# Performance work log

Hardware: AMD Instinct MI355X
Metric: run time of the kernel (lower is better)

## Reference

```python
import jax, jax.numpy as jnp
import numpy as np

B, L, D, H, R = 2, 2048, 1024, 16, 512
HD = D // H  # head dim = 64
EPS = 1e-5


def layernorm(x, g, b):
    mu = jnp.mean(x, axis=-1, keepdims=True)
    var = jnp.mean(jnp.square(x - mu), axis=-1, keepdims=True)
    return (x - mu) * jax.lax.rsqrt(var + EPS) * g + b


def rel_pos_bias(res_pos, size):
    # Equivalent to the torch 'skew' causal_mask: bias[h, i, j] = res_pos[h, i-j]
    # if 0 <= i-j < R else -inf (causal + clipped relative distance).
    d = jnp.arange(size)[:, None] - jnp.arange(size)[None, :]  # (L, L)
    valid = (d >= 0) & (d < res_pos.shape[-1])
    gathered = res_pos[:, jnp.clip(d, 0, res_pos.shape[-1] - 1)]  # (H, L, L)
    return jnp.where(valid, gathered, -jnp.inf)


def setup_inputs() -> dict:
    key = jax.random.key(0)
    ks = jax.random.split(key, 12)
    s = lambda fan: 1.0 / np.sqrt(fan)
    return {
        "x": jax.random.normal(ks[0], (B, L, D), jnp.float32),
        "res_pos": jax.random.normal(ks[1], (H, R), jnp.float32) * 0.02,
        "w_qkv": jax.random.normal(ks[2], (D, 3 * D), jnp.float32) * s(D),
        "b_qkv": jnp.zeros((3 * D,), jnp.float32),
        "w_out": jax.random.normal(ks[3], (D, D), jnp.float32) * s(D),
        "b_out": jnp.zeros((D,), jnp.float32),
        "w1": jax.random.normal(ks[4], (D, 4 * D), jnp.float32) * s(D),
        "b1": jnp.zeros((4 * D,), jnp.float32),
        "w2": jax.random.normal(ks[5], (4 * D, D), jnp.float32) * s(4 * D),
        "b2": jnp.zeros((D,), jnp.float32),
        "ln1_g": jnp.ones((D,), jnp.float32),
        "ln1_b": jnp.zeros((D,), jnp.float32),
        "ln2_g": jnp.ones((D,), jnp.float32),
        "ln2_b": jnp.zeros((D,), jnp.float32),
    }


def reference(x, res_pos, w_qkv, b_qkv, w_out, b_out, w1, b1, w2, b2,
              ln1_g, ln1_b, ln2_g, ln2_b):
    b, l, _ = x.shape
    xn = layernorm(x, ln1_g, ln1_b)  # pre-norm
    qkv = xn @ w_qkv + b_qkv  # (B, L, 3D)
    q, k, v = jnp.split(qkv, 3, axis=-1)
    # (B, H, L, HD)
    q = q.reshape(b, l, H, HD).transpose(0, 2, 1, 3)
    k = k.reshape(b, l, H, HD).transpose(0, 2, 1, 3)
    v = v.reshape(b, l, H, HD).transpose(0, 2, 1, 3)
    scale = 1.0 / np.sqrt(HD)
    scores = jnp.einsum('bhqd,bhkd->bhqk', q, k) * scale
    scores = scores + rel_pos_bias(res_pos, l)[None]  # additive rel-pos causal mask
    attn = jax.nn.softmax(scores, axis=-1)
    ctx = jnp.einsum('bhqk,bhkd->bhqd', attn, v)
    ctx = ctx.transpose(0, 2, 1, 3).reshape(b, l, D)
    x = x + ctx @ w_out + b_out  # residual 1
    h = layernorm(x, ln2_g, ln2_b)
    h = jax.nn.relu(h @ w1 + b1) @ w2 + b2
    return x + h  # residual 2
```

## Files before the change

kernel.cpp:

```cpp
#include <hip/hip_runtime.h>
#include <math.h>

#define B_  2
#define L_  2048
#define D_  1024
#define H_  16
#define R_  512
#define HD_ 64
#define M_  (B_*L_)
#define EPS_ 1e-5f

typedef __attribute__((ext_vector_type(8))) short bf16x8;
typedef __attribute__((ext_vector_type(4))) float f32x4;

__device__ __forceinline__ unsigned short f2bf(float f) {
    unsigned int u = __float_as_uint(f);
    u += 0x7fffu + ((u >> 16) & 1u);
    return (unsigned short)(u >> 16);
}

__device__ __forceinline__ void gl2lds16(const void* g, void* l) {
    __builtin_amdgcn_global_load_lds(
        (const __attribute__((address_space(1))) unsigned int*)g,
        (__attribute__((address_space(3))) unsigned int*)l, 16, 0, 0);
}

__global__ __launch_bounds__(256) void ln_kernel(const float* __restrict__ x,
                                                 const float* __restrict__ g,
                                                 const float* __restrict__ b,
                                                 unsigned short* __restrict__ out) {
    int row = blockIdx.x;
    int t = threadIdx.x;
    const float4* xr = (const float4*)(x + (size_t)row * D_);
    float4 v = xr[t];
    float s  = v.x + v.y + v.z + v.w;
    float ss = v.x*v.x + v.y*v.y + v.z*v.z + v.w*v.w;
    #pragma unroll
    for (int o = 32; o > 0; o >>= 1) {
        s  += __shfl_down(s,  o);
        ss += __shfl_down(ss, o);
    }
    __shared__ float rs[4], rss[4];
    int wave = t >> 6, lane = t & 63;
    if (lane == 0) { rs[wave] = s; rss[wave] = ss; }
    __syncthreads();
    if (t == 0) {
        float a = 0.f, c = 0.f;
        for (int i = 0; i < 4; i++) { a += rs[i]; c += rss[i]; }
        rs[0] = a; rss[0] = c;
    }
    __syncthreads();
    float mean = rs[0] * (1.0f / D_);
    float var  = rss[0] * (1.0f / D_) - mean * mean;
    float inv  = rsqrtf(var + EPS_);
    float4 gv = ((const float4*)g)[t];
    float4 bv = ((const float4*)b)[t];
    ushort4 ob;
    ob.x = f2bf((v.x - mean) * inv * gv.x + bv.x);
    ob.y = f2bf((v.y - mean) * inv * gv.y + bv.y);
    ob.z = f2bf((v.z - mean) * inv * gv.z + bv.z);
    ob.w = f2bf((v.w - mean) * inv * gv.w + bv.w);
    ((ushort4*)(out + (size_t)row * D_))[t] = ob;
}

__global__ __launch_bounds__(256) void wtrans_kernel(const float* __restrict__ in,
                                                     unsigned short* __restrict__ out,
                                                     int K, int N) {
    __shared__ float tile[32][33];
    int bn = blockIdx.x * 32, bk = blockIdx.y * 32;
    int t = threadIdx.x;
    int r = t >> 3, c4 = (t & 7) * 4;
    float4 v = *(const float4*)(in + (size_t)(bk + r) * N + bn + c4);
    tile[r][c4+0] = v.x; tile[r][c4+1] = v.y; tile[r][c4+2] = v.z; tile[r][c4+3] = v.w;
    __syncthreads();
    ushort4 o;
    o.x = f2bf(tile[c4+0][r]);
    o.y = f2bf(tile[c4+1][r]);
    o.z = f2bf(tile[c4+2][r]);
    o.w = f2bf(tile[c4+3][r]);
    *(ushort4*)(out + (size_t)(bn + r) * K + bk + c4) = o;
}

template<int BM, int KSPLIT, int RELU, int OUT_BF16>
__global__ __launch_bounds__(256) void gemm_mfma(const unsigned short* __restrict__ A,
                                                 const unsigned short* __restrict__ Wt,
                                                 const float* __restrict__ bias,
                                                 const float* __restrict__ res,
                                                 void* __restrict__ Cout,
                                                 int M, int N, int K) {
    constexpr int BN = 128;
    constexpr int BK = KSPLIT * 32;
    constexpr int TM = BM / 32;
    __shared__ __align__(16) unsigned short As[KSPLIT * BM * 32];
    __shared__ __align__(16) unsigned short Bs[KSPLIT * BN * 32];
    int t = threadIdx.x;
    int wave = t >> 6, lane = t & 63;
    int q = lane >> 4, cl = lane & 15;
    int bm = blockIdx.x * BM, bn = blockIdx.y * BN;
    int wm = (wave >> 1) * (BM / 2);
    int wn = (wave & 1) * 64;

    int sm = t >> 2;
    int sc = (t & 3) * 8;

    f32x4 acc[TM][4] = {};

    for (int kt = 0; kt < K; kt += BK) {
        __syncthreads();
        #pragma unroll
        for (int hh = 0; hh < KSPLIT; hh++) {
            #pragma unroll
            for (int s = 0; s < BM / 64; s++)
                gl2lds16(A + (size_t)(bm + s*64 + sm) * K + kt + hh*32 + sc,
                         &As[hh * BM * 32 + (s*64 + sm) * 32 + sc]);
            #pragma unroll
            for (int s = 0; s < 2; s++)
                gl2lds16(Wt + (size_t)(bn + s*64 + sm) * K + kt + hh*32 + sc,
                         &Bs[hh * BN * 32 + (s*64 + sm) * 32 + sc]);
        }
        __syncthreads();

        #pragma unroll
        for (int hh = 0; hh < KSPLIT; hh++) {
            bf16x8 af[TM], bfr[4];
            #pragma unroll
            for (int i = 0; i < TM; i++)
                af[i] = *(const bf16x8*)&As[hh * BM * 32 + (wm + i*16 + cl) * 32 + q*8];
            #pragma unroll
            for (int j = 0; j < 4; j++)
                bfr[j] = *(const bf16x8*)&Bs[hh * BN * 32 + (wn + j*16 + cl) * 32 + q*8];
            #pragma unroll
            for (int i = 0; i < TM; i++)
                #pragma unroll
                for (int j = 0; j < 4; j++)
                    acc[i][j] = __builtin_amdgcn_mfma_f32_16x16x32_bf16(
                                    af[i], bfr[j], acc[i][j], 0, 0, 0);
        }
    }

    #pragma unroll
    for (int i = 0; i < TM; i++) {
        #pragma unroll
        for (int j = 0; j < 4; j++) {
            #pragma unroll
            for (int r = 0; r < 4; r++) {
                int row = bm + wm + i*16 + q*4 + r;
                int col = bn + wn + j*16 + cl;
                float v = acc[i][j][r] + bias[col];
                if (RELU) v = fmaxf(v, 0.0f);
                if (res)  v += res[(size_t)row * N + col];
                if (OUT_BF16)
                    ((unsigned short*)Cout)[(size_t)row * N + col] = f2bf(v);
                else
                    ((float*)Cout)[(size_t)row * N + col] = v;
            }
        }
    }
}

#define AP_ 80
__global__ __launch_bounds__(256) void attn_mfma_kernel(const unsigned short* __restrict__ qkv,
                                                        const float* __restrict__ res_pos,
                                                        unsigned short* __restrict__ ctx) {
    int q0 = blockIdx.x * 64;
    int h  = blockIdx.y;
    int b  = blockIdx.z;
    int t  = threadIdx.x;
    int w  = t >> 6, lane = t & 63;
    int quad = lane >> 4, cl = lane & 15;

    __shared__ __align__(16) unsigned short sQP[64 * AP_];
    __shared__ __align__(16) unsigned short sK [64 * AP_];
    __shared__ __align__(16) unsigned short sVt[64 * AP_];
    __shared__ float sBias[R_];

    const int bL = b * L_;
    const unsigned short* base = qkv + (size_t)bL * 3072;

    #pragma unroll
    for (int c = t; c < 512; c += 256) {
        int row = c >> 3, off = (c & 7) * 8;
        uint4 v = *(const uint4*)(base + (size_t)(q0 + row) * 3072 + h * HD_ + off);
        *(uint4*)&sQP[row * AP_ + off] = v;
    }
    sBias[t]       = res_pos[h * R_ + t];
    sBias[t + 256] = res_pos[h * R_ + t + 256];
    __syncthreads();

    bf16x8 qf0 = *(const bf16x8*)&sQP[(w*16 + cl) * AP_ + quad*8];
    bf16x8 qf1 = *(const bf16x8*)&sQP[(w*16 + cl) * AP_ + 32 + quad*8];

    f32x4 accO[4] = {};
    float m_i[4], l_i[4];
    #pragma unroll
    for (int r = 0; r < 4; r++) { m_i[r] = -1e30f; l_i[r] = 0.f; }

    int klo = q0 - (R_ - 1); if (klo < 0) klo = 0;
    int kt0 = klo & ~63;
    const float scale = 0.125f;

    for (int k0 = kt0; k0 <= q0; k0 += 64) {
        __syncthreads();
        #pragma unroll
        for (int c = t; c < 512; c += 256) {
            int row = c >> 3, off = (c & 7) * 8;
            uint4 v = *(const uint4*)(base + (size_t)(k0 + row) * 3072 + D_ + h * HD_ + off);
            *(uint4*)&sK[row * AP_ + off] = v;
        }
        {
            int kp = t & 31, dg = t >> 5;
            const unsigned short* v0 = base + (size_t)(k0 + 2*kp) * 3072 + 2*D_ + h * HD_ + dg*8;
            uint4 a4 = *(const uint4*)v0;
            uint4 b4 = *(const uint4*)(v0 + 3072);
            const unsigned short* pa = (const unsigned short*)&a4;
            const unsigned short* pb = (const unsigned short*)&b4;
            #pragma unroll
            for (int i = 0; i < 8; i++) {
                unsigned int packed = (unsigned int)pa[i] | ((unsigned int)pb[i] << 16);
                *(unsigned int*)&sVt[(dg*8 + i) * AP_ + 2*kp] = packed;
            }
        }
        __syncthreads();

        f32x4 sacc[4] = {};
        #pragma unroll
        for (int j = 0; j < 4; j++) {
            bf16x8 kf0 = *(const bf16x8*)&sK[(j*16 + cl) * AP_ + quad*8];
            bf16x8 kf1 = *(const bf16x8*)&sK[(j*16 + cl) * AP_ + 32 + quad*8];
            sacc[j] = __builtin_amdgcn_mfma_f32_16x16x32_bf16(qf0, kf0, sacc[j], 0, 0, 0);
            sacc[j] = __builtin_amdgcn_mfma_f32_16x16x32_bf16(qf1, kf1, sacc[j], 0, 0, 0);
        }

        float alpha[4];
        #pragma unroll
        for (int r = 0; r < 4; r++) {
            int qrow = q0 + w*16 + quad*4 + r;
            float sv[4];
            float rm = -1e30f;
            #pragma unroll
            for (int j = 0; j < 4; j++) {
                int key = k0 + j*16 + cl;
                int diff = qrow - key;
                bool valid = ((unsigned)diff) < (unsigned)R_;
                int dc = valid ? diff : 0;
                float x = fmaf(sacc[j][r], scale, sBias[dc]);
                sv[j] = valid ? x : -1e30f;
                rm = fmaxf(rm, sv[j]);
            }
            #pragma unroll
            for (int o = 8; o > 0; o >>= 1) rm = fmaxf(rm, __shfl_xor(rm, o));
            float mnew = fmaxf(m_i[r], rm);
            alpha[r] = __expf(m_i[r] - mnew);
            m_i[r] = mnew;
            float rsum = 0.f;
            #pragma unroll
            for (int j = 0; j < 4; j++) {
                float p = (sv[j] > -1e29f) ? __expf(sv[j] - mnew) : 0.f;
                sv[j] = p;
                rsum += p;
            }
            #pragma unroll
            for (int o = 8; o > 0; o >>= 1) rsum += __shfl_xor(rsum, o);
            l_i[r] = l_i[r] * alpha[r] + rsum;
            #pragma unroll
            for (int j = 0; j < 4; j++)
                sQP[(w*16 + quad*4 + r) * AP_ + j*16 + cl] = f2bf(sv[j]);
        }
        #pragma unroll
        for (int j = 0; j < 4; j++)
            #pragma unroll
            for (int r = 0; r < 4; r++)
                accO[j][r] *= alpha[r];
        __syncthreads();

        bf16x8 pf0 = *(const bf16x8*)&sQP[(w*16 + cl) * AP_ + quad*8];
        bf16x8 pf1 = *(const bf16x8*)&sQP[(w*16 + cl) * AP_ + 32 + quad*8];
        #pragma unroll
        for (int j = 0; j < 4; j++) {
            bf16x8 vf0 = *(const bf16x8*)&sVt[(j*16 + cl) * AP_ + quad*8];
            bf16x8 vf1 = *(const bf16x8*)&sVt[(j*16 + cl) * AP_ + 32 + quad*8];
            accO[j] = __builtin_amdgcn_mfma_f32_16x16x32_bf16(pf0, vf0, accO[j], 0, 0, 0);
            accO[j] = __builtin_amdgcn_mfma_f32_16x16x32_bf16(pf1, vf1, accO[j], 0, 0, 0);
        }
    }

    #pragma unroll
    for (int r = 0; r < 4; r++) {
        float inv = 1.0f / l_i[r];
        int row = bL + q0 + w*16 + quad*4 + r;
        #pragma unroll
        for (int j = 0; j < 4; j++)
            ctx[(size_t)row * D_ + h * HD_ + j*16 + cl] = f2bf(accO[j][r] * inv);
    }
}

extern "C" void kernel_launch(void* const* d_in, const int* in_sizes, int n_in,
                              void* d_out, int out_size, void* d_ws, size_t ws_size,
                              hipStream_t stream) {
    const float* x      = (const float*)d_in[0];
    const float* res_pos= (const float*)d_in[1];
    const float* w_qkv  = (const float*)d_in[2];
    const float* b_qkv  = (const float*)d_in[3];
    const float* w_out  = (const float*)d_in[4];
    const float* b_out  = (const float*)d_in[5];
    const float* w1     = (const float*)d_in[6];
    const float* b1     = (const float*)d_in[7];
    const float* w2     = (const float*)d_in[8];
    const float* b2     = (const float*)d_in[9];
    const float* ln1_g  = (const float*)d_in[10];
    const float* ln1_b  = (const float*)d_in[11];
    const float* ln2_g  = (const float*)d_in[12];
    const float* ln2_b  = (const float*)d_in[13];
    float* out = (float*)d_out;
    char* ws = (char*)d_ws;

    unsigned short* act_bf = (unsigned short*)ws;
    unsigned short* wqkvT  = (unsigned short*)(ws + ((size_t)8  << 20));
    unsigned short* woutT  = (unsigned short*)(ws + ((size_t)14 << 20));
    unsigned short* w1T    = (unsigned short*)(ws + ((size_t)16 << 20));
    unsigned short* w2T    = (unsigned short*)(ws + ((size_t)24 << 20));
    unsigned short* qkv_bf = (unsigned short*)(ws + ((size_t)32 << 20));
    unsigned short* h1_bf  = (unsigned short*)(ws + ((size_t)32 << 20));

    wtrans_kernel<<<dim3(3072/32, 1024/32), 256, 0, stream>>>(w_qkv, wqkvT, 1024, 3072);
    wtrans_kernel<<<dim3(1024/32, 1024/32), 256, 0, stream>>>(w_out, woutT, 1024, 1024);
    wtrans_kernel<<<dim3(4096/32, 1024/32), 256, 0, stream>>>(w1,   w1T,   1024, 4096);
    wtrans_kernel<<<dim3(1024/32, 4096/32), 256, 0, stream>>>(w2,   w2T,   4096, 1024);

    ln_kernel<<<M_, 256, 0, stream>>>(x, ln1_g, ln1_b, act_bf);
    gemm_mfma<128,1,0,1><<<dim3(M_/128, 3072/128), 256, 0, stream>>>(
        act_bf, wqkvT, b_qkv, nullptr, qkv_bf, M_, 3072, 1024);
    attn_mfma_kernel<<<dim3(L_/64, H_, B_), 256, 0, stream>>>(qkv_bf, res_pos, act_bf);
    gemm_mfma<64,1,0,0><<<dim3(M_/64, 1024/128), 256, 0, stream>>>(
        act_bf, woutT, b_out, x, out, M_, 1024, 1024);
    ln_kernel<<<M_, 256, 0, stream>>>(out, ln2_g, ln2_b, act_bf);
    gemm_mfma<128,1,1,1><<<dim3(M_/128, 4096/128), 256, 0, stream>>>(
        act_bf, w1T, b1, nullptr, h1_bf, M_, 4096, 1024);
    gemm_mfma<64,2,0,0><<<dim3(M_/64, 1024/128), 256, 0, stream>>>(
        h1_bf, w2T, b2, out, out, M_, 1024, 4096);
}
```

Baseline: 367.7 us.

## Split-K the FFN down-projection GEMM and double the K-step of the other GEMMs

The w2 GEMM (K=4096) is split into two K halves along blockIdx.z. Each half writes fp32 partials to separate workspace buffers, and a new reduce kernel sums them with the bias and the residual into the output. This doubles the block count for a GEMM that previously launched only 512 blocks. The other three GEMMs switch to KSPLIT=2, which loads 64-wide K tiles per sync. The workspace is rearranged so one partial buffer reuses the region of weights already consumed, at the cost of extra fp32 partial traffic and one more kernel launch.

```diff
diff --git a/kernel.cpp b/kernel.cpp
--- a/kernel.cpp
+++ b/kernel.cpp
@@ -81,12 +81,13 @@
     *(ushort4*)(out + (size_t)(bn + r) * K + bk + c4) = o;
 }
 
-template<int BM, int KSPLIT, int RELU, int OUT_BF16>
+template<int BM, int KSPLIT, int SPLITK, int RELU, int OUT_BF16>
 __global__ __launch_bounds__(256) void gemm_mfma(const unsigned short* __restrict__ A,
                                                  const unsigned short* __restrict__ Wt,
                                                  const float* __restrict__ bias,
                                                  const float* __restrict__ res,
                                                  void* __restrict__ Cout,
+                                                 void* __restrict__ Cout2,
                                                  int M, int N, int K) {
     constexpr int BN = 128;
     constexpr int BK = KSPLIT * 32;
@@ -103,9 +104,13 @@
     int sm = t >> 2;
     int sc = (t & 3) * 8;
 
+    int kchunk = K / SPLITK;
+    int kbase  = (SPLITK > 1) ? blockIdx.z * kchunk : 0;
+    void* Cptr = (SPLITK > 1 && blockIdx.z == 1) ? Cout2 : Cout;
+
     f32x4 acc[TM][4] = {};
 
-    for (int kt = 0; kt < K; kt += BK) {
+    for (int kt = kbase; kt < kbase + kchunk; kt += BK) {
         __syncthreads();
         #pragma unroll
         for (int hh = 0; hh < KSPLIT; hh++) {
@@ -146,16 +151,35 @@
             for (int r = 0; r < 4; r++) {
                 int row = bm + wm + i*16 + q*4 + r;
                 int col = bn + wn + j*16 + cl;
-                float v = acc[i][j][r] + bias[col];
+                float v = acc[i][j][r];
+                if (bias) v += bias[col];
                 if (RELU) v = fmaxf(v, 0.0f);
                 if (res)  v += res[(size_t)row * N + col];
                 if (OUT_BF16)
-                    ((unsigned short*)Cout)[(size_t)row * N + col] = f2bf(v);
+                    ((unsigned short*)Cptr)[(size_t)row * N + col] = f2bf(v);
                 else
-                    ((float*)Cout)[(size_t)row * N + col] = v;
+                    ((float*)Cptr)[(size_t)row * N + col] = v;
             }
         }
     }
+}
+
+__global__ __launch_bounds__(256) void reduce_splitk_kernel(const float* __restrict__ p0,
+                                                            const float* __restrict__ p1,
+                                                            const float* __restrict__ bias,
+                                                            float* __restrict__ out) {
+    size_t g = (size_t)blockIdx.x * 256 + threadIdx.x;
+    int col4 = (int)(g & 255);
+    float4 a = ((const float4*)p0)[g];
+    float4 b = ((const float4*)p1)[g];
+    float4 c = ((float4*)out)[g];
+    float4 bv = ((const float4*)bias)[col4];
+    float4 o;
+    o.x = c.x + a.x + b.x + bv.x;
+    o.y = c.y + a.y + b.y + bv.y;
+    o.z = c.z + a.z + b.z + bv.z;
+    o.w = c.w + a.w + b.w + bv.w;
+    ((float4*)out)[g] = o;
 }
 
 #define AP_ 80
@@ -315,12 +339,14 @@
     char* ws = (char*)d_ws;
 
     unsigned short* act_bf = (unsigned short*)ws;
-    unsigned short* wqkvT  = (unsigned short*)(ws + ((size_t)8  << 20));
-    unsigned short* woutT  = (unsigned short*)(ws + ((size_t)14 << 20));
-    unsigned short* w1T    = (unsigned short*)(ws + ((size_t)16 << 20));
-    unsigned short* w2T    = (unsigned short*)(ws + ((size_t)24 << 20));
+    unsigned short* w2T    = (unsigned short*)(ws + ((size_t)8  << 20));
+    unsigned short* wqkvT  = (unsigned short*)(ws + ((size_t)16 << 20));
+    unsigned short* woutT  = (unsigned short*)(ws + ((size_t)22 << 20));
+    unsigned short* w1T    = (unsigned short*)(ws + ((size_t)24 << 20));
     unsigned short* qkv_bf = (unsigned short*)(ws + ((size_t)32 << 20));
     unsigned short* h1_bf  = (unsigned short*)(ws + ((size_t)32 << 20));
+    float*          part0  = (float*)         (ws + ((size_t)64 << 20));
+    float*          part1  = (float*)         (ws + ((size_t)16 << 20));
 
     wtrans_kernel<<<dim3(3072/32, 1024/32), 256, 0, stream>>>(w_qkv, wqkvT, 1024, 3072);
     wtrans_kernel<<<dim3(1024/32, 1024/32), 256, 0, stream>>>(w_out, woutT, 1024, 1024);
@@ -328,14 +354,15 @@
     wtrans_kernel<<<dim3(1024/32, 4096/32), 256, 0, stream>>>(w2,   w2T,   4096, 1024);
 
     ln_kernel<<<M_, 256, 0, stream>>>(x, ln1_g, ln1_b, act_bf);
-    gemm_mfma<128,1,0,1><<<dim3(M_/128, 3072/128), 256, 0, stream>>>(
-        act_bf, wqkvT, b_qkv, nullptr, qkv_bf, M_, 3072, 1024);
+    gemm_mfma<128,2,1,0,1><<<dim3(M_/128, 3072/128), 256, 0, stream>>>(
+        act_bf, wqkvT, b_qkv, nullptr, qkv_bf, nullptr, M_, 3072, 1024);
     attn_mfma_kernel<<<dim3(L_/64, H_, B_), 256, 0, stream>>>(qkv_bf, res_pos, act_bf);
-    gemm_mfma<64,1,0,0><<<dim3(M_/64, 1024/128), 256, 0, stream>>>(
-        act_bf, woutT, b_out, x, out, M_, 1024, 1024);
+    gemm_mfma<64,2,1,0,0><<<dim3(M_/64, 1024/128), 256, 0, stream>>>(
+        act_bf, woutT, b_out, x, out, nullptr, M_, 1024, 1024);
     ln_kernel<<<M_, 256, 0, stream>>>(out, ln2_g, ln2_b, act_bf);
-    gemm_mfma<128,1,1,1><<<dim3(M_/128, 4096/128), 256, 0, stream>>>(
-        act_bf, w1T, b1, nullptr, h1_bf, M_, 4096, 1024);
-    gemm_mfma<64,2,0,0><<<dim3(M_/64, 1024/128), 256, 0, stream>>>(
-        h1_bf, w2T, b2, out, out, M_, 1024, 4096);
-}
+    gemm_mfma<128,2,1,1,1><<<dim3(M_/128, 4096/128), 256, 0, stream>>>(
+        act_bf, w1T, b1, nullptr, h1_bf, nullptr, M_, 4096, 1024);
+    gemm_mfma<64,2,2,0,0><<<dim3(M_/64, 1024/128, 2), 256, 0, stream>>>(
+        h1_bf, w2T, nullptr, nullptr, part0, part1, M_, 1024, 4096);
+    reduce_splitk_kernel<<<(M_ * D_ / 4) / 256, 256, 0, stream>>>(part0, part1, b2, out);
+}
```

After: 400.7 us. 1.09x slower.
